# Optimization experiments

Measured on AMD Instinct MI355X. Metric: run time of the kernel, lower is better.

The kernel has to match this reference:

```python
import jax, jax.numpy as jnp
import numpy as np

EPS = 1e-5  # torch LayerNorm default


def _ln(x, g, b):
    mu = jnp.mean(x, axis=-1, keepdims=True)
    var = jnp.var(x, axis=-1, keepdims=True)
    return (x - mu) * jax.lax.rsqrt(var + EPS) * g + b


def _linear(x, w, b):
    # torch nn.Linear: y = x @ W^T + b, W is [out, in]
    return jnp.einsum('bnc,dc->bnd', x, w) + b


def setup_inputs() -> dict:
    key = jax.random.key(0)
    ks = jax.random.split(key, 12)
    B, C, H, W = 16, 768, 32, 32
    s = 1.0 / np.sqrt(C)
    inp = {
        'x_rgb': jax.random.normal(ks[0], (B, C, H, W), jnp.float32),
        'x_tir': jax.random.normal(ks[1], (B, C, H, W), jnp.float32),
        'x_before': jax.random.normal(ks[2], (B, C, H, W), jnp.float32),
        'w0': jax.random.uniform(ks[3], (C, C), jnp.float32, -s, s),
        'b0': jax.random.uniform(ks[4], (C,), jnp.float32, -s, s),
        'w1': jax.random.uniform(ks[5], (C, C), jnp.float32, -s, s),
        'b1': jax.random.uniform(ks[6], (C,), jnp.float32, -s, s),
        'w2': jax.random.uniform(ks[7], (C, C), jnp.float32, -s, s),
        'b2': jax.random.uniform(ks[8], (C,), jnp.float32, -s, s),
        'ln_g': jnp.ones((C,), jnp.float32),
        'ln_b': jnp.zeros((C,), jnp.float32),
        'wp': jax.random.uniform(ks[9], (C, C), jnp.float32, -s, s),
        'bp': jax.random.uniform(ks[10], (C,), jnp.float32, -s, s),
    }
    return inp


def reference(x_rgb, x_tir, x_before, w0, b0, w1, b1, w2, b2, ln_g, ln_b, wp, bp):
    B, C, H, W = x_rgb.shape
    N = H * W
    scale = C ** (-0.5)
    # flatten(2).permute(0,2,1): [B,C,H,W] -> [B, N, C]
    to_tok = lambda x: jnp.transpose(x.reshape(B, C, N), (0, 2, 1))
    r = _linear(_ln(to_tok(x_rgb), ln_g, ln_b), w0, b0)
    t = _linear(_ln(to_tok(x_tir), ln_g, ln_b), w1, b1)
    f = _linear(_ln(to_tok(x_before), ln_g, ln_b), w2, b2)
    x_sum = r + t
    x_mul = r * t
    # attention: [B, N, N]
    attn = jax.nn.softmax(jnp.einsum('bnc,bmc->bnm', r, f) * scale, axis=-1)
    mid = jnp.einsum('bnm,bmc->bnc', attn, t)
    # faithful to torch: .transpose(1,2).reshape(B, N, C) (element reorder)
    mid = jnp.transpose(mid, (0, 2, 1)).reshape(B, N, C)
    x_middle = x_sum + mid
    x_middle = x_middle + _linear(_ln(x_middle, ln_g, ln_b), wp, bp)
    res = jax.nn.gelu(x_sum, approximate=False) * x_middle \
        + jax.nn.gelu(x_mul, approximate=False) * x_middle
    return res.reshape(B, C, H, W)
```

## Files before the change

kernel.cpp:

```cpp
#include <hip/hip_runtime.h>
#include <hip/hip_bf16.h>
#include <math.h>

typedef unsigned short u16;
typedef __attribute__((ext_vector_type(8))) short bf16x8;
typedef __attribute__((ext_vector_type(4))) float f32x4;
typedef __attribute__((ext_vector_type(4))) u16 u16x4;

#define DEVI static __device__ __forceinline__

DEVI float bf2f(u16 h){ union{unsigned u; float f;} v; v.u=((unsigned)h)<<16; return v.f; }
DEVI u16 f2bf(float x){ union{float f; unsigned u;} v; v.f=x; unsigned r=v.u+0x7fffu+((v.u>>16)&1u); return (u16)(r>>16); }
DEVI void split2(float x, u16 &h, u16 &l){ h=f2bf(x); l=f2bf(x-bf2f(h)); }
DEVI float geluf(float x){ return 0.5f*x*(1.0f+erff(x*0.70710678118654752f)); }

#define GLD16(g,s) __builtin_amdgcn_global_load_lds((const __attribute__((address_space(1))) void*)(g), (__attribute__((address_space(3))) void*)(s), 16, 0, 0)

__global__ void ln_part_k(const float* __restrict__ x0, const float* __restrict__ x1,
                          const float* __restrict__ x2, float* __restrict__ sP,
                          float* __restrict__ s2P)
{
  const int inp = blockIdx.y;
  const float* x = inp==0?x0:(inp==1?x1:x2);
  const int tile = blockIdx.x>>3, chunk = blockIdx.x&7;
  const int T0 = tile*256;
  const int b = T0>>10, n0 = T0&1023;
  const int tid = threadIdx.x, lane = tid&63, part = tid>>6;
  const float* base = x + ((size_t)b*768 + chunk*96)*1024 + n0 + lane*4;
  float4 s = {0,0,0,0}, s2 = {0,0,0,0};
  for (int c=part; c<96; c+=4){
    float4 v = *(const float4*)(base + (size_t)c*1024);
    s.x+=v.x; s.y+=v.y; s.z+=v.z; s.w+=v.w;
    s2.x+=v.x*v.x; s2.y+=v.y*v.y; s2.z+=v.z*v.z; s2.w+=v.w*v.w;
  }
  __shared__ float4 L1[4][64], L2[4][64];
  L1[part][lane]=s; L2[part][lane]=s2;
  __syncthreads();
  const float* f1=(const float*)L1; const float* f2=(const float*)L2;
  float a  = f1[tid]+f1[256+tid]+f1[512+tid]+f1[768+tid];
  float a2 = f2[tid]+f2[256+tid]+f2[512+tid]+f2[768+tid];
  long o = (long)inp*131072 + (long)chunk*16384 + T0 + tid;
  sP[o]=a; s2P[o]=a2;
}

__global__ void ln_fin_k(const float* __restrict__ sP, const float* __restrict__ s2P,
                         float* __restrict__ muS, float* __restrict__ rsS)
{
  int i = blockIdx.x*256+threadIdx.x;
  int inp = i>>14, ti = i&16383;
  long base = (long)inp*131072 + ti;
  float s=0.f, s2=0.f;
  #pragma unroll
  for (int k=0;k<8;k++){ s += sP[base+(long)k*16384]; s2 += s2P[base+(long)k*16384]; }
  float mu = s*(1.f/768.f);
  float var = s2*(1.f/768.f)-mu*mu;
  muS[i]=mu; rsS[i]=rsqrtf(var+1e-5f);
}

__global__ void ln_apply_k(const float* __restrict__ x, const float* __restrict__ muS,
                           const float* __restrict__ rsS, const float* __restrict__ g,
                           const float* __restrict__ be, u16* __restrict__ Ah,
                           u16* __restrict__ Al, int inp)
{
  const int b = blockIdx.y;
  const int gx = blockIdx.x;
  const int c0=(gx%24)*32, n0=(gx/24)*32;
  const int tid=threadIdx.x;
  __shared__ u16 Hh[32][33], Hl[32][33];
  const int nl=tid&31, cp=tid>>5;
  const int tok = b*1024 + n0 + nl;
  const float mu = muS[inp*16384+tok], rs = rsS[inp*16384+tok];
  #pragma unroll
  for (int i=0;i<4;i++){
    int cl = cp + i*8;
    int c = c0 + cl;
    float v = x[((size_t)(b*768+c))*1024 + n0 + nl];
    float y = (v-mu)*rs*g[c]+be[c];
    u16 h,l; split2(y,h,l);
    Hh[cl][nl]=h; Hl[cl][nl]=l;
  }
  __syncthreads();
  const int wn = tid>>3, wc=(tid&7)*4;
  u16x4 vh, vl;
  #pragma unroll
  for (int j=0;j<4;j++){ vh[j]=Hh[wc+j][wn]; vl[j]=Hl[wc+j][wn]; }
  size_t o = ((size_t)(b*1024+n0+wn))*768 + c0 + wc;
  *(u16x4*)(Ah+o)=vh; *(u16x4*)(Al+o)=vl;
}

__global__ void wsplit_k(const float* __restrict__ w0,const float* __restrict__ w1,
                         const float* __restrict__ w2,const float* __restrict__ wpk,
                         u16* __restrict__ wh, u16* __restrict__ wl)
{
  const int ws = blockIdx.y;
  const float* w = ws==0?w0:(ws==1?w1:(ws==2?w2:wpk));
  int i = blockIdx.x*256+threadIdx.x;
  u16 h,l; split2(w[i],h,l);
  wh[(size_t)ws*589824+i]=h; wl[(size_t)ws*589824+i]=l;
}

__global__ void tr_pairs_k(const u16* __restrict__ Sh, const u16* __restrict__ Sl,
                           u16* __restrict__ Dh, u16* __restrict__ Dl)
{
  const int b = blockIdx.y;
  const int gx = blockIdx.x;
  const int c0=(gx%24)*32, n0=(gx/24)*32;
  const int tid=threadIdx.x;
  __shared__ u16 Th[32][33], Tl[32][33];
  const int cl=tid&31, np=tid>>5;
  #pragma unroll
  for (int i=0;i<4;i++){
    int nl = np + i*8;
    size_t o = ((size_t)(b*1024+n0+nl))*768 + c0 + cl;
    Th[cl][nl]=Sh[o]; Tl[cl][nl]=Sl[o];
  }
  __syncthreads();
  const int nl2=tid&31, cp2=tid>>5;
  #pragma unroll
  for (int i=0;i<4;i++){
    int cl2 = cp2 + i*8;
    size_t o = ((size_t)b*786432) + (size_t)(c0+cl2)*1024 + n0 + nl2;
    Dh[o]=Th[cl2][nl2]; Dl[o]=Tl[cl2][nl2];
  }
}

__global__ void softmax_k(float* __restrict__ S)
{
  const long row = blockIdx.x;
  const int tid=threadIdx.x;
  const int lane=tid&63, wid=tid>>6;
  float4 v4 = *(const float4*)(S + row*1024 + tid*4);
  float m = fmaxf(fmaxf(v4.x,v4.y),fmaxf(v4.z,v4.w));
  for (int o=1;o<64;o<<=1) m = fmaxf(m, __shfl_xor(m,o,64));
  __shared__ float red[4]; __shared__ float red2[4];
  if (lane==0) red[wid]=m;
  __syncthreads();
  m = fmaxf(fmaxf(red[0],red[1]),fmaxf(red[2],red[3]));
  float e0=__expf(v4.x-m), e1=__expf(v4.y-m), e2=__expf(v4.z-m), e3=__expf(v4.w-m);
  float s = e0+e1+e2+e3;
  for (int o=1;o<64;o<<=1) s += __shfl_xor(s,o,64);
  if (lane==0) red2[wid]=s;
  __syncthreads();
  s = red2[0]+red2[1]+red2[2]+red2[3];
  float inv = 1.f/s;
  u16x4 h4,l4;
  u16 h,l;
  split2(e0*inv,h,l); h4[0]=h; l4[0]=l;
  split2(e1*inv,h,l); h4[1]=h; l4[1]=l;
  split2(e2*inv,h,l); h4[2]=h; l4[2]=l;
  split2(e3*inv,h,l); h4[3]=h; l4[3]=l;
  u16* base = (u16*)S + row*2048;
  *(u16x4*)(base + tid*4)        = h4;
  *(u16x4*)(base + 1024 + tid*4) = l4;
}

__global__ void ln_rows_k(const float* __restrict__ x, const float* __restrict__ g,
                          const float* __restrict__ be, u16* __restrict__ Oh, u16* __restrict__ Ol)
{
  const long row=blockIdx.x;
  const int tid=threadIdx.x;
  const float* xr = x + row*768;
  float v0=xr[tid], v1=xr[tid+256], v2=xr[tid+512];
  float s=v0+v1+v2, s2=v0*v0+v1*v1+v2*v2;
  for (int o=1;o<64;o<<=1){ s+=__shfl_xor(s,o,64); s2+=__shfl_xor(s2,o,64); }
  __shared__ float rA[4]; __shared__ float rB[4];
  const int lane=tid&63, wid=tid>>6;
  if(lane==0){rA[wid]=s;rB[wid]=s2;}
  __syncthreads();
  s=rA[0]+rA[1]+rA[2]+rA[3]; s2=rB[0]+rB[1]+rB[2]+rB[3];
  float mu=s*(1.f/768.f), var=s2*(1.f/768.f)-mu*mu, rs=rsqrtf(var+1e-5f);
  u16 h,l;
  float y0=(v0-mu)*rs*g[tid]+be[tid];         split2(y0,h,l); Oh[row*768+tid]=h;     Ol[row*768+tid]=l;
  float y1=(v1-mu)*rs*g[tid+256]+be[tid+256]; split2(y1,h,l); Oh[row*768+tid+256]=h; Ol[row*768+tid+256]=l;
  float y2=(v2-mu)*rs*g[tid+512]+be[tid+512]; split2(y2,h,l); Oh[row*768+tid+512]=h; Ol[row*768+tid+512]=l;
}

template<int EPI>
__launch_bounds__(256,2)
__global__ void gemm3_k(const u16* __restrict__ Ah, const u16* __restrict__ Al, long aBat, int lda,
                        const u16* __restrict__ Bh, const u16* __restrict__ Bl, long bBat, int ldb,
                        int K, int tilesM, int ldo, long oBat, float scaleV,
                        const float* __restrict__ bias,
                        u16* __restrict__ Oh, u16* __restrict__ Ol,
                        float* __restrict__ outF,
                        const float* __restrict__ xmid,
                        const u16* __restrict__ rhp, const u16* __restrict__ rlp,
                        const u16* __restrict__ thp, const u16* __restrict__ tlp,
                        float* __restrict__ dout)
{
  __shared__ u16 sm[16384];
  u16* sAh=sm; u16* sAl=sm+4096; u16* sBh=sm+8192; u16* sBl=sm+12288;
  const int tid=threadIdx.x, lane=tid&63, wid=tid>>6;
  const int wm=(wid&1)*64, wn=(wid>>1)*64;
  const int tm = (blockIdx.x % tilesM)*128;
  const int tn = (blockIdx.x / tilesM)*128;
  const int batch = blockIdx.y;
  const u16* gAh = Ah + (long)batch*aBat + (long)tm*lda;
  const u16* gAl = Al + (long)batch*aBat + (long)tm*lda;
  const u16* gBh = Bh + (long)batch*bBat + (long)tn*ldb;
  const u16* gBl = Bl + (long)batch*bBat + (long)tn*ldb;
  f32x4 acc[4][4];
  #pragma unroll
  for(int i=0;i<4;i++)
    #pragma unroll
    for(int j=0;j<4;j++) acc[i][j]=(f32x4){0.f,0.f,0.f,0.f};
  const int frow=lane&15, fko=(lane>>4)<<3;
  const int nkt=K>>5;
  for(int kt=0;kt<nkt;kt++){
    const int k0=kt<<5;
    __syncthreads();
    #pragma unroll
    for(int is=0;is<2;is++){
      int idx=is*256+tid;
      int mm=idx>>2, ko=(idx&3)<<3;
      long goA=(long)mm*lda + k0 + ko;
      long goB=(long)mm*ldb + k0 + ko;
      int so=(idx & ~63)*8;
      GLD16(gAh+goA, sAh+so);
      GLD16(gAl+goA, sAl+so);
      GLD16(gBh+goB, sBh+so);
      GLD16(gBl+goB, sBl+so);
    }
    __syncthreads();
    bf16x8 fbh[4], fbl[4];
    #pragma unroll
    for(int j=0;j<4;j++){
      int off=(wn+j*16+frow)*32+fko;
      fbh[j]=*(const bf16x8*)(sBh+off);
      fbl[j]=*(const bf16x8*)(sBl+off);
    }
    #pragma unroll
    for(int i=0;i<4;i++){
      int off=(wm+i*16+frow)*32+fko;
      bf16x8 fah=*(const bf16x8*)(sAh+off);
      bf16x8 fal=*(const bf16x8*)(sAl+off);
      #pragma unroll
      for(int j=0;j<4;j++){
        acc[i][j]=__builtin_amdgcn_mfma_f32_16x16x32_bf16(fah,fbh[j],acc[i][j],0,0,0);
        acc[i][j]=__builtin_amdgcn_mfma_f32_16x16x32_bf16(fah,fbl[j],acc[i][j],0,0,0);
        acc[i][j]=__builtin_amdgcn_mfma_f32_16x16x32_bf16(fal,fbh[j],acc[i][j],0,0,0);
      }
    }
  }
  const int r0 = tm+wm+((lane>>4)<<2);
  const int c0 = tn+wn+(lane&15);
  #pragma unroll
  for(int i=0;i<4;i++){
    #pragma unroll
    for(int q=0;q<4;q++){
      int r = r0 + i*16 + q;
      #pragma unroll
      for(int j=0;j<4;j++){
        int cc = c0 + j*16;
        float v = acc[i][j][q];
        if constexpr (EPI==4){
          long o2 = (long)batch*oBat + (long)cc*1024 + (r&1023);
          float rv = bf2f(rhp[o2])+bf2f(rlp[o2]);
          float tv = bf2f(thp[o2])+bf2f(tlp[o2]);
          outF[o2] = (rv+tv)+v;
        } else {
          long o = (long)batch*oBat + (long)(r>>10)*oBat + (long)(r&1023)*ldo + cc;
          if constexpr (EPI==0){
            v += bias[cc];
            u16 h,l; split2(v,h,l);
            Oh[o]=h; Ol[o]=l;
          } else if constexpr (EPI==1){
            outF[o] = v*scaleV;
          } else if constexpr (EPI==2){
            outF[o] = v;
          } else {
            float lin = v + bias[cc];
            float xmv = xmid[o];
            float rv = bf2f(rhp[o])+bf2f(rlp[o]);
            float tv = bf2f(thp[o])+bf2f(tlp[o]);
            float xs=rv+tv, xmu=rv*tv;
            dout[o] = (geluf(xs)+geluf(xmu))*(xmv+lin);
          }
        }
      }
    }
  }
}

extern "C" void kernel_launch(void* const* d_in, const int* in_sizes, int n_in,
                              void* d_out, int out_size, void* d_ws, size_t ws_size,
                              hipStream_t stream)
{
  const float* x_rgb=(const float*)d_in[0];
  const float* x_tir=(const float*)d_in[1];
  const float* x_bef=(const float*)d_in[2];
  const float* w0=(const float*)d_in[3];
  const float* b0=(const float*)d_in[4];
  const float* w1=(const float*)d_in[5];
  const float* b1=(const float*)d_in[6];
  const float* w2=(const float*)d_in[7];
  const float* b2=(const float*)d_in[8];
  const float* lng=(const float*)d_in[9];
  const float* lnb=(const float*)d_in[10];
  const float* wpk=(const float*)d_in[11];
  const float* bp=(const float*)d_in[12];
  float* out=(float*)d_out;

  char* wsb=(char*)d_ws;
  size_t off=0;
  auto alloc=[&](size_t bytes)->char*{ char* p=wsb+off; off=(off+bytes+255)&~(size_t)255; return p; };

  const long PAIRE = (long)16384*768;
  float* muS = (float*)alloc(3*16384*4);
  float* rsS = (float*)alloc(3*16384*4);
  float* sP  = (float*)alloc((size_t)3*8*16384*4);
  float* s2P = (float*)alloc((size_t)3*8*16384*4);
  u16* wh = (u16*)alloc(4*589824*2);
  u16* wl = (u16*)alloc(4*589824*2);
  char* stageA = alloc((size_t)2*PAIRE*2);
  u16* sAh=(u16*)stageA;      u16* sAl=sAh+PAIRE;
  u16* tTh=sAh;               u16* tTl=sAh+PAIRE;
  u16* xmh=sAh;               u16* xml=sAh+PAIRE;
  u16* rh=(u16*)alloc(PAIRE*2); u16* rl=(u16*)alloc(PAIRE*2);
  u16* th=(u16*)alloc(PAIRE*2); u16* tl=(u16*)alloc(PAIRE*2);
  char* fmid = alloc((size_t)2*PAIRE*2);
  u16* fb=(u16*)fmid;
  float* midf=(float*)fmid;
  char* SPx = alloc((size_t)8*1024*1024*4);
  float* Sf=(float*)SPx;
  u16* Pu=(u16*)SPx;

  if (off > ws_size){
    hipMemsetAsync(d_out, 0, (size_t)out_size*4, stream);
    return;
  }

  const float SC = 0.03608439182435161f;
  dim3 blk(256);

  wsplit_k<<<dim3(2304,4),blk,0,stream>>>(w0,w1,w2,wpk,wh,wl);
  ln_part_k<<<dim3(512,3),blk,0,stream>>>(x_rgb,x_tir,x_bef,sP,s2P);
  ln_fin_k<<<dim3(192),blk,0,stream>>>(sP,s2P,muS,rsS);

  ln_apply_k<<<dim3(768,16),blk,0,stream>>>(x_rgb,muS,rsS,lng,lnb,sAh,sAl,0);
  gemm3_k<0><<<dim3(128*6,1),blk,0,stream>>>(sAh,sAl,0,768, wh,wl,0,768, 768,128,768,786432, 0.f,
      b0, rh,rl, nullptr, nullptr,nullptr,nullptr,nullptr,nullptr,nullptr);
  ln_apply_k<<<dim3(768,16),blk,0,stream>>>(x_tir,muS,rsS,lng,lnb,sAh,sAl,1);
  gemm3_k<0><<<dim3(128*6,1),blk,0,stream>>>(sAh,sAl,0,768, wh+589824,wl+589824,0,768, 768,128,768,786432, 0.f,
      b1, th,tl, nullptr, nullptr,nullptr,nullptr,nullptr,nullptr,nullptr);
  ln_apply_k<<<dim3(768,16),blk,0,stream>>>(x_bef,muS,rsS,lng,lnb,sAh,sAl,2);
  gemm3_k<0><<<dim3(128*6,1),blk,0,stream>>>(sAh,sAl,0,768, wh+2*589824,wl+2*589824,0,768, 768,128,768,1572864, 0.f,
      b2, fb,fb+786432, nullptr, nullptr,nullptr,nullptr,nullptr,nullptr,nullptr);

  tr_pairs_k<<<dim3(768,16),blk,0,stream>>>(th,tl,tTh,tTl);

  for (int c=0;c<2;c++){
    long cb = (long)c*8;
    gemm3_k<1><<<dim3(8*8,8),blk,0,stream>>>(rh+cb*786432,rl+cb*786432,786432,768,
        fb+cb*1572864,fb+786432+cb*1572864,1572864,768,
        768,8,1024,1048576, SC, nullptr, nullptr,nullptr, Sf,
        nullptr,nullptr,nullptr,nullptr,nullptr,nullptr);
    softmax_k<<<dim3(8192),blk,0,stream>>>(Sf);
    gemm3_k<4><<<dim3(8*6,8),blk,0,stream>>>(Pu,Pu+1024,2097152,2048,
        tTh+cb*786432,tTl+cb*786432,786432,1024,
        1024,8,1024,786432, 0.f, nullptr, nullptr,nullptr, midf+cb*786432,
        nullptr, rh+cb*786432,rl+cb*786432, th+cb*786432,tl+cb*786432, nullptr);
  }

  ln_rows_k<<<dim3(16384),blk,0,stream>>>(midf,lng,lnb,xmh,xml);
  gemm3_k<3><<<dim3(128*6,1),blk,0,stream>>>(xmh,xml,0,768, wh+3*589824,wl+3*589824,0,768,
      768,128,768,786432, 0.f, bp, nullptr,nullptr, nullptr, midf, rh,rl,th,tl, out);
}
```

Measured before the change: 892.5 us.

## Double-buffer LDS tiles and XOR-swizzle k-chunks in the split-bf16 GEMM

The GEMM kernel now keeps two LDS stages. It issues the global-to-LDS loads for the next k-tile before computing on the current one, which removes one barrier per iteration and overlaps load latency with MFMA work. It also XOR-swizzles the 16-byte k-chunk position within each LDS row, both when staging and when reading fragments, to reduce LDS bank conflicts on the fragment reads. The cost is double the LDS per block (64 KB), which may limit occupancy under the 2-block launch bound.

```diff
diff --git a/kernel.cpp b/kernel.cpp
--- a/kernel.cpp
+++ b/kernel.cpp
@@ -188,8 +188,7 @@
                         const u16* __restrict__ thp, const u16* __restrict__ tlp,
                         float* __restrict__ dout)
 {
-  __shared__ u16 sm[16384];
-  u16* sAh=sm; u16* sAl=sm+4096; u16* sBh=sm+8192; u16* sBl=sm+12288;
+  __shared__ u16 sm[2][16384];
   const int tid=threadIdx.x, lane=tid&63, wid=tid>>6;
   const int wm=(wid&1)*64, wn=(wid>>1)*64;
   const int tm = (blockIdx.x % tilesM)*128;
@@ -199,39 +198,49 @@
   const u16* gAl = Al + (long)batch*aBat + (long)tm*lda;
   const u16* gBh = Bh + (long)batch*bBat + (long)tn*ldb;
   const u16* gBl = Bl + (long)batch*bBat + (long)tn*ldb;
-  f32x4 acc[4][4];
-  #pragma unroll
-  for(int i=0;i<4;i++)
-    #pragma unroll
-    for(int j=0;j<4;j++) acc[i][j]=(f32x4){0.f,0.f,0.f,0.f};
-  const int frow=lane&15, fko=(lane>>4)<<3;
-  const int nkt=K>>5;
-  for(int kt=0;kt<nkt;kt++){
-    const int k0=kt<<5;
-    __syncthreads();
+
+  auto STAGE=[&](u16* dst, int k0){
     #pragma unroll
     for(int is=0;is<2;is++){
       int idx=is*256+tid;
-      int mm=idx>>2, ko=(idx&3)<<3;
-      long goA=(long)mm*lda + k0 + ko;
-      long goB=(long)mm*ldb + k0 + ko;
+      int mm=idx>>2;
+      int c = (idx&3) ^ ((mm>>1)&3);
+      long goA=(long)mm*lda + k0 + (c<<3);
+      long goB=(long)mm*ldb + k0 + (c<<3);
       int so=(idx & ~63)*8;
-      GLD16(gAh+goA, sAh+so);
-      GLD16(gAl+goA, sAl+so);
-      GLD16(gBh+goB, sBh+so);
-      GLD16(gBl+goB, sBl+so);
+      GLD16(gAh+goA, dst+so);
+      GLD16(gAl+goA, dst+4096+so);
+      GLD16(gBh+goB, dst+8192+so);
+      GLD16(gBl+goB, dst+12288+so);
     }
+  };
+
+  f32x4 acc[4][4];
+  #pragma unroll
+  for(int i=0;i<4;i++)
+    #pragma unroll
+    for(int j=0;j<4;j++) acc[i][j]=(f32x4){0.f,0.f,0.f,0.f};
+  const int frow=lane&15, slotc=lane>>4;
+  const int nkt=K>>5;
+
+  STAGE(sm[0], 0);
+  int cur=0;
+  for(int kt=0;kt<nkt;kt++){
     __syncthreads();
+    if(kt+1<nkt) STAGE(sm[cur^1], (kt+1)<<5);
+    u16* sAh=sm[cur]; u16* sAl=sAh+4096; u16* sBh=sAh+8192; u16* sBl=sAh+12288;
     bf16x8 fbh[4], fbl[4];
     #pragma unroll
     for(int j=0;j<4;j++){
-      int off=(wn+j*16+frow)*32+fko;
+      int srow=wn+j*16+frow;
+      int off=srow*32 + ((slotc ^ ((srow>>1)&3))<<3);
       fbh[j]=*(const bf16x8*)(sBh+off);
       fbl[j]=*(const bf16x8*)(sBl+off);
     }
     #pragma unroll
     for(int i=0;i<4;i++){
-      int off=(wm+i*16+frow)*32+fko;
+      int srow=wm+i*16+frow;
+      int off=srow*32 + ((slotc ^ ((srow>>1)&3))<<3);
       bf16x8 fah=*(const bf16x8*)(sAh+off);
       bf16x8 fal=*(const bf16x8*)(sAl+off);
       #pragma unroll
@@ -241,7 +250,9 @@
         acc[i][j]=__builtin_amdgcn_mfma_f32_16x16x32_bf16(fal,fbh[j],acc[i][j],0,0,0);
       }
     }
-  }
+    cur^=1;
+  }
+
   const int r0 = tm+wm+((lane>>4)<<2);
   const int c0 = tn+wn+(lane&15);
   #pragma unroll
```

Measured after the change: 977.4 us. +9.5%, slower.
